# Performance work log

Hardware: AMD Instinct MI355X
Metric: run time of the kernel (lower is better)

Reference implementation:

```python
import jax, jax.numpy as jnp
import numpy as np

N_TOKEN = 267735
HEAD = 20000
CUTOFFS = [20000, 20008, 20016, 200000, 267735]  # from cl_root_leaf_dict with 2 roots of 8 leaves
N_ROOTS = 2


def setup_inputs() -> dict:
    key = jax.random.key(0)
    k1, k2, k3, k4 = jax.random.split(key, 4)
    N, D = 1024, 1024
    hidden = jax.random.normal(k1, (N, D), dtype=jnp.float32)
    target = jax.random.randint(k2, (N,), 0, N_TOKEN)
    W = jax.random.normal(k3, (N_TOKEN, D), dtype=jnp.float32) * 0.02
    b = jnp.zeros((N_TOKEN,), dtype=jnp.float32)
    cluster_weight = jax.random.normal(k4, (2, D), dtype=jnp.float32) * 0.02
    cluster_bias = jnp.zeros((2,), dtype=jnp.float32)
    return {"hidden": hidden, "target": target, "W": W, "b": b,
            "cluster_weight": cluster_weight, "cluster_bias": cluster_bias}


def _nll(hidden, target, W, b, cw, cb):
    cutoff_ends = [0] + CUTOFFS
    # head = first 20000 vocab rows + 2 cluster rows (d_proj == d_embed -> no projection)
    head_w = jnp.concatenate([W[:HEAD], cw], axis=0)          # [20002, D]
    head_b = jnp.concatenate([b[:HEAD], cb], axis=0)          # [20002]
    head_lp = jax.nn.log_softmax(hidden @ head_w.T + head_b, axis=-1)  # [N, 20002]
    n_head_cols = head_lp.shape[1]
    rows = jnp.arange(hidden.shape[0])
    # segment 0: target in [0, 20000) -> nll directly from head log-probs
    lp0 = head_lp[rows, jnp.clip(target, 0, HEAD - 1)]
    nll = -lp0  # only valid where target < HEAD; overwritten below otherwise
    for i in range(1, len(CUTOFFS)):
        l, r = cutoff_ends[i], cutoff_ends[i + 1]
        # per-segment tail logits for all tokens (masked combine keeps shapes static)
        tail_lp = jax.nn.log_softmax(hidden @ W[l:r].T + b[l:r], axis=-1)  # [N, r-l]
        # routing column exactly as in the torch code:
        # j = i-1 for root segments, -(i - n_roots) for the two cluster segments
        j = (i - 1) if i <= N_ROOTS else (n_head_cols - (i - N_ROOTS))
        lp_i = head_lp[:, j] + tail_lp[rows, jnp.clip(target - l, 0, r - l - 1)]
        mask = (target >= l) & (target < r)
        nll = jnp.where(mask, -lp_i, nll)
    return nll


def reference(hidden, target, W, b, cluster_weight, cluster_bias):
    return _nll(hidden, target, W, b, cluster_weight, cluster_bias)
```

## Files before the change

### kernel.cpp

```cpp
#include <hip/hip_runtime.h>
#include <hip/hip_bf16.h>

#define D_DIM 1024
#define NTOK 267735
#define NEXT_ 267737
#define HEADN 20000

typedef __attribute__((ext_vector_type(8))) short bf16x8;
typedef __attribute__((ext_vector_type(4))) float f32x4;

__device__ __forceinline__ int seg_of(int c){
  if (c < HEADN)  return 0;
  if (c < 20008)  return 1;
  if (c < 20016)  return 2;
  if (c < 200000) return 3;
  if (c < NTOK)   return 4;
  return 0;
}

__device__ __forceinline__ unsigned pack2(float x, float y){
  __hip_bfloat16 a = __float2bfloat16(x);
  __hip_bfloat16 b = __float2bfloat16(y);
  unsigned short ua = *reinterpret_cast<unsigned short*>(&a);
  unsigned short ub = *reinterpret_cast<unsigned short*>(&b);
  return (unsigned)ua | ((unsigned)ub << 16);
}

#define BM 256
#define BN 128
#define BK 32
#define NTHREADS 512

__device__ __forceinline__ int swz_w(int r, int k4){
  int c = (k4 >> 1) ^ ((r >> 1) & 3);
  return r*32 + c*8 + (k4 & 1)*4;
}
__device__ __forceinline__ int swz_r(int row, int q){
  return row*32 + ((q ^ ((row >> 1) & 3)) << 3);
}

__global__ __launch_bounds__(NTHREADS, 1) void gemm_lse_kernel(
    const float* __restrict__ hidden, const float* __restrict__ W,
    const float* __restrict__ bias,   const float* __restrict__ cw,
    const float* __restrict__ cb,     float* __restrict__ accg)
{
  __shared__ unsigned short lsA[BM * 32];
  __shared__ unsigned short lsB[BN * 32];

  const int tid = threadIdx.x;
  const int rowBase = blockIdx.x * BM;
  const int colBase = blockIdx.y * BN;

  const float* aSrc[4]; int aRow[4], aK4[4];
#pragma unroll
  for (int i=0;i<4;++i){
    int idx = tid + NTHREADS*i;
    aRow[i] = idx >> 3; aK4[i] = idx & 7;
    aSrc[i] = hidden + (size_t)(rowBase + aRow[i]) * D_DIM + aK4[i]*4;
  }
  const float* bSrc[2]; int bRow[2], bK4[2];
#pragma unroll
  for (int i=0;i<2;++i){
    int idx = tid + NTHREADS*i;
    bRow[i] = idx >> 3; bK4[i] = idx & 7;
    int c = colBase + bRow[i];
    const float* base;
    if (c < NTOK)       base = W  + (size_t)c * D_DIM;
    else if (c < NEXT_) base = cw + (size_t)(c - NTOK) * D_DIM;
    else                base = W;
    bSrc[i] = base + bK4[i]*4;
  }

  const int lane = tid & 63;
  const int wv = tid >> 6;
  const int wm = wv >> 1;
  const int wn = wv & 1;
  const int q  = lane >> 4;
  const int r16 = lane & 15;

  f32x4 acc[4][4];
#pragma unroll
  for (int i=0;i<4;++i)
#pragma unroll
    for (int j=0;j<4;++j) acc[i][j] = (f32x4){0.f,0.f,0.f,0.f};

  for (int kt = 0; kt < D_DIM/BK; ++kt){
    float4 av[4], bv[2];
#pragma unroll
    for (int i=0;i<4;++i) av[i] = *reinterpret_cast<const float4*>(aSrc[i] + kt*BK);
#pragma unroll
    for (int i=0;i<2;++i) bv[i] = *reinterpret_cast<const float4*>(bSrc[i] + kt*BK);
    __syncthreads();
#pragma unroll
    for (int i=0;i<4;++i){
      unsigned* p = reinterpret_cast<unsigned*>(&lsA[swz_w(aRow[i], aK4[i])]);
      p[0] = pack2(av[i].x, av[i].y); p[1] = pack2(av[i].z, av[i].w);
    }
#pragma unroll
    for (int i=0;i<2;++i){
      unsigned* p = reinterpret_cast<unsigned*>(&lsB[swz_w(bRow[i], bK4[i])]);
      p[0] = pack2(bv[i].x, bv[i].y); p[1] = pack2(bv[i].z, bv[i].w);
    }
    __syncthreads();
    bf16x8 afr[4], bfr[4];
#pragma unroll
    for (int f=0; f<4; ++f) afr[f] = *reinterpret_cast<const bf16x8*>(&lsA[swz_r(wm*64 + f*16 + r16, q)]);
#pragma unroll
    for (int f=0; f<4; ++f) bfr[f] = *reinterpret_cast<const bf16x8*>(&lsB[swz_r(wn*64 + f*16 + r16, q)]);
#pragma unroll
    for (int i=0;i<4;++i)
#pragma unroll
      for (int j=0;j<4;++j)
        acc[i][j] = __builtin_amdgcn_mfma_f32_16x16x32_bf16(afr[i], bfr[j], acc[i][j], 0, 0, 0);
  }

  int sq[4]; float bq[4];
#pragma unroll
  for (int f=0; f<4; ++f){
    int c = colBase + wn*64 + f*16 + r16;
    if (c < NTOK)       { sq[f] = seg_of(c); bq[f] = bias[c]; }
    else if (c < NEXT_) { sq[f] = 0;         bq[f] = cb[c - NTOK]; }
    else                { sq[f] = -1;        bq[f] = 0.f; }
  }
  int sfirst = seg_of(colBase);
  int clast  = colBase + BN - 1; if (clast > NEXT_-1) clast = NEXT_-1;
  int slast  = seg_of(clast);
  int smin = sfirst, smax = slast;
  if (slast < sfirst){ smin = 0; smax = 4; }

#pragma unroll
  for (int i=0;i<4;++i){
#pragma unroll
    for (int r=0;r<4;++r){
      float e[4];
#pragma unroll
      for (int f=0;f<4;++f) e[f] = __expf(acc[i][f][r] + bq[f]);
      int rowg = rowBase + wm*64 + i*16 + (lane>>4)*4 + r;
      for (int s = smin; s <= smax; ++s){
        float p = 0.f;
#pragma unroll
        for (int f=0;f<4;++f) p += (sq[f]==s) ? e[f] : 0.f;
#pragma unroll
        for (int off=1; off<16; off<<=1) p += __shfl_xor(p, off, 16);
        if ((lane & 15) == 0 && p != 0.f) atomicAdd(&accg[rowg*8 + s], p);
      }
    }
  }
}

__global__ __launch_bounds__(256) void finalize_kernel(
    const float* __restrict__ hidden, const int* __restrict__ target,
    const float* __restrict__ W,      const float* __restrict__ bias,
    const float* __restrict__ cw,     const float* __restrict__ cb,
    const float* __restrict__ accg,   float* __restrict__ out)
{
  const int row  = blockIdx.x * 4 + (threadIdx.x >> 6);
  const int lane = threadIdx.x & 63;
  const int t = target[row];

  const float4* h4 = reinterpret_cast<const float4*>(hidden + (size_t)row * D_DIM);
  const float4* w1 = reinterpret_cast<const float4*>(W + (size_t)t * D_DIM);
  int s = 0; const float* jraw = W; float jb = 0.f;
  if (t >= HEADN){
    if      (t < 20008)  { s=1; jraw = W;          jb = bias[0]; }
    else if (t < 20016)  { s=2; jraw = W + D_DIM;  jb = bias[1]; }
    else if (t < 200000) { s=3; jraw = cw + D_DIM; jb = cb[1];   }
    else                 { s=4; jraw = cw;         jb = cb[0];   }
  }
  const float4* w2 = reinterpret_cast<const float4*>(jraw);

  float p1 = 0.f, p2 = 0.f;
#pragma unroll
  for (int j=0;j<4;++j){
    float4 hv = h4[lane + 64*j];
    float4 av = w1[lane + 64*j];
    float4 bv = w2[lane + 64*j];
    p1 += hv.x*av.x + hv.y*av.y + hv.z*av.z + hv.w*av.w;
    p2 += hv.x*bv.x + hv.y*bv.y + hv.z*bv.z + hv.w*bv.w;
  }
#pragma unroll
  for (int off=32; off; off>>=1){
    p1 += __shfl_xor(p1, off, 64);
    p2 += __shfl_xor(p2, off, 64);
  }

  if (lane == 0){
    float lseH = __logf(accg[row*8 + 0]);
    float nll;
    if (t < HEADN){
      nll = -(p1 + bias[t] - lseH);
    } else {
      float lseS = __logf(accg[row*8 + s]);
      nll = -((p2 + jb - lseH) + (p1 + bias[t] - lseS));
    }
    out[row] = nll;
  }
}

extern "C" void kernel_launch(void* const* d_in, const int* in_sizes, int n_in,
                              void* d_out, int out_size, void* d_ws, size_t ws_size,
                              hipStream_t stream)
{
  const float* hidden = (const float*)d_in[0];
  const int*   target = (const int*)  d_in[1];
  const float* W      = (const float*)d_in[2];
  const float* bias   = (const float*)d_in[3];
  const float* cw     = (const float*)d_in[4];
  const float* cb     = (const float*)d_in[5];
  float* out  = (float*)d_out;
  float* accg = (float*)d_ws;

  hipMemsetAsync(accg, 0, 1024*8*sizeof(float), stream);

  dim3 grid(1024/BM, (NEXT_ + BN - 1)/BN);
  gemm_lse_kernel<<<grid, NTHREADS, 0, stream>>>(hidden, W, bias, cw, cb, accg);
  finalize_kernel<<<256, 256, 0, stream>>>(hidden, target, W, bias, cw, cb, accg, out);
}
```

Measured before the change: 984.4 us.

## Double-buffer LDS tiles with register prefetch and raise occupancy hint

The GEMM main loop now uses two LDS buffers and two sets of staging registers. Global loads for the next K-step are issued before the current tile is converted and stored, which removes one barrier per K-step and overlaps memory latency with MFMA work. The launch bound also changes from 1 to 4 blocks per CU, which tightens the register budget. With 64 accumulator floats per thread plus prefetch registers, that tighter budget risks spilling. The doubled LDS footprint may also prevent the requested occupancy from being reached.

New measurement: 1.713 ms. 1.74x slower.

```diff
diff --git a/kernel.cpp b/kernel.cpp
--- a/kernel.cpp
+++ b/kernel.cpp
@@ -30,6 +30,7 @@
 #define BN 128
 #define BK 32
 #define NTHREADS 512
+#define KSTEPS (D_DIM/BK)
 
 __device__ __forceinline__ int swz_w(int r, int k4){
   int c = (k4 >> 1) ^ ((r >> 1) & 3);
@@ -39,13 +40,15 @@
   return row*32 + ((q ^ ((row >> 1) & 3)) << 3);
 }
 
-__global__ __launch_bounds__(NTHREADS, 1) void gemm_lse_kernel(
+__global__ __launch_bounds__(NTHREADS, 4) void gemm_lse_kernel(
     const float* __restrict__ hidden, const float* __restrict__ W,
     const float* __restrict__ bias,   const float* __restrict__ cw,
     const float* __restrict__ cb,     float* __restrict__ accg)
 {
-  __shared__ unsigned short lsA[BM * 32];
-  __shared__ unsigned short lsB[BN * 32];
+  __shared__ unsigned short lsA0[BM * 32];
+  __shared__ unsigned short lsB0[BN * 32];
+  __shared__ unsigned short lsA1[BM * 32];
+  __shared__ unsigned short lsB1[BN * 32];
 
   const int tid = threadIdx.x;
   const int rowBase = blockIdx.x * BM;
@@ -84,34 +87,53 @@
 #pragma unroll
     for (int j=0;j<4;++j) acc[i][j] = (f32x4){0.f,0.f,0.f,0.f};
 
-  for (int kt = 0; kt < D_DIM/BK; ++kt){
-    float4 av[4], bv[2];
+  float4 rA0[4], rB0[2], rA1[4], rB1[2];
+
+  auto do_load_a = [&](float4* av, int kt){
 #pragma unroll
     for (int i=0;i<4;++i) av[i] = *reinterpret_cast<const float4*>(aSrc[i] + kt*BK);
+  };
+  auto do_load_b = [&](float4* bv, int kt){
 #pragma unroll
     for (int i=0;i<2;++i) bv[i] = *reinterpret_cast<const float4*>(bSrc[i] + kt*BK);
-    __syncthreads();
+  };
+  auto do_store = [&](unsigned short* LA, unsigned short* LB, const float4* av, const float4* bv){
 #pragma unroll
     for (int i=0;i<4;++i){
-      unsigned* p = reinterpret_cast<unsigned*>(&lsA[swz_w(aRow[i], aK4[i])]);
+      unsigned* p = reinterpret_cast<unsigned*>(&LA[swz_w(aRow[i], aK4[i])]);
       p[0] = pack2(av[i].x, av[i].y); p[1] = pack2(av[i].z, av[i].w);
     }
 #pragma unroll
     for (int i=0;i<2;++i){
-      unsigned* p = reinterpret_cast<unsigned*>(&lsB[swz_w(bRow[i], bK4[i])]);
+      unsigned* p = reinterpret_cast<unsigned*>(&LB[swz_w(bRow[i], bK4[i])]);
       p[0] = pack2(bv[i].x, bv[i].y); p[1] = pack2(bv[i].z, bv[i].w);
     }
-    __syncthreads();
+  };
+  auto do_mfma = [&](const unsigned short* LA, const unsigned short* LB){
     bf16x8 afr[4], bfr[4];
 #pragma unroll
-    for (int f=0; f<4; ++f) afr[f] = *reinterpret_cast<const bf16x8*>(&lsA[swz_r(wm*64 + f*16 + r16, q)]);
-#pragma unroll
-    for (int f=0; f<4; ++f) bfr[f] = *reinterpret_cast<const bf16x8*>(&lsB[swz_r(wn*64 + f*16 + r16, q)]);
+    for (int f=0; f<4; ++f) afr[f] = *reinterpret_cast<const bf16x8*>(&LA[swz_r(wm*64 + f*16 + r16, q)]);
+#pragma unroll
+    for (int f=0; f<4; ++f) bfr[f] = *reinterpret_cast<const bf16x8*>(&LB[swz_r(wn*64 + f*16 + r16, q)]);
 #pragma unroll
     for (int i=0;i<4;++i)
 #pragma unroll
       for (int j=0;j<4;++j)
         acc[i][j] = __builtin_amdgcn_mfma_f32_16x16x32_bf16(afr[i], bfr[j], acc[i][j], 0, 0, 0);
+  };
+
+  do_load_a(rA0, 0); do_load_b(rB0, 0);
+
+  for (int kt2 = 0; kt2 < KSTEPS/2; ++kt2){
+    const int k0 = kt2*2;
+    do_load_a(rA1, k0+1); do_load_b(rB1, k0+1);
+    do_store(lsA0, lsB0, rA0, rB0);
+    __syncthreads();
+    do_mfma(lsA0, lsB0);
+    if (kt2 < KSTEPS/2 - 1){ do_load_a(rA0, k0+2); do_load_b(rB0, k0+2); }
+    do_store(lsA1, lsB1, rA1, rB1);
+    __syncthreads();
+    do_mfma(lsA1, lsB1);
   }
 
   int sq[4]; float bq[4];
```
